# Optimization experiments

Measured on AMD Instinct MI355X. Metric: run time of the kernel, lower is better.

Reference implementation:

```python
import jax, jax.numpy as jnp
import numpy as np

N_HEADS = 12


def setup_inputs() -> dict:
    key = jax.random.key(0)
    ks = jax.random.split(key, 4)
    B, T, C = 1, 4096, 768
    x = jax.random.normal(ks[0], (B, T, C), dtype=jnp.float32)
    w_qkv = jax.random.normal(ks[1], (C, 3 * C), dtype=jnp.float32) * (C ** -0.5)
    b_qkv = jnp.zeros((3 * C,), dtype=jnp.float32)
    w_proj = jax.random.normal(ks[2], (C, C), dtype=jnp.float32) * (C ** -0.5)
    b_proj = jnp.zeros((C,), dtype=jnp.float32)
    return {"x": x, "w_qkv": w_qkv, "b_qkv": b_qkv, "w_proj": w_proj, "b_proj": b_proj}


def reference(x, w_qkv, b_qkv, w_proj, b_proj):
    B, T, C = x.shape
    H = N_HEADS
    hd = C // H
    qkv = x @ w_qkv + b_qkv                      # [B,T,3C]
    q, k, v = jnp.split(qkv, 3, axis=-1)
    # [B,H,T,hd]
    q = q.reshape(B, T, H, hd).transpose(0, 2, 1, 3)
    k = k.reshape(B, T, H, hd).transpose(0, 2, 1, 3)
    v = v.reshape(B, T, H, hd).transpose(0, 2, 1, 3)
    scale = 1.0 / jnp.sqrt(jnp.float32(hd))
    attn = jnp.einsum('bhqd,bhkd->bhqk', q, k) * scale  # [B,H,T,T]
    causal = jnp.tril(jnp.ones((T, T), dtype=bool))
    attn = jnp.where(causal, attn, jnp.float32(-jnp.inf))
    attn = jax.nn.softmax(attn, axis=-1)
    out = jnp.einsum('bhqk,bhkd->bhqd', attn, v)        # [B,H,T,hd]
    out = out.transpose(0, 2, 1, 3).reshape(B, T, C)
    return out @ w_proj + b_proj
```

## Files before the change

### kernel.cpp

```cpp
#include <hip/hip_runtime.h>
#include <hip/hip_bf16.h>


#define T_SEQ 4096
#define C_DIM 768
#define C3    2304
#define NH    12
#define HD    64

typedef __attribute__((ext_vector_type(8))) short bf16x8;
typedef __attribute__((ext_vector_type(4))) short bf16x4;
typedef __attribute__((ext_vector_type(4))) float f32x4;

__device__ inline unsigned short f2bf(float f) {
  union { float f; unsigned u; } v; v.f = f;
  unsigned r = v.u + 0x7fff + ((v.u >> 16) & 1);
  return (unsigned short)(r >> 16);
}
__device__ inline unsigned short f2bf_trunc(float f) {
  union { float f; unsigned u; } v; v.f = f;
  return (unsigned short)(v.u >> 16);
}

__device__ inline void gl2lds16(const void* g, void* l) {
  __builtin_amdgcn_global_load_lds(
      (const __attribute__((address_space(1))) unsigned int*)g,
      (__attribute__((address_space(3))) unsigned int*)l, 16, 0, 0);
}

#if __has_builtin(__builtin_amdgcn_exp2f)
#define EXP2F(x) __builtin_amdgcn_exp2f(x)
#else
#define EXP2F(x) exp2f(x)
#endif

#define NB_CONV  (T_SEQ * C_DIM / 2048)
#define NB_TQKV  ((C3 / 32) * (C_DIM / 32))
#define NB_TPROJ ((C_DIM / 32) * (C_DIM / 32))

__global__ __launch_bounds__(256) void prep_fused(
    const float* __restrict__ x, const float* __restrict__ w_qkv,
    const float* __restrict__ w_proj, unsigned short* __restrict__ xb,
    unsigned short* __restrict__ wqkvT, unsigned short* __restrict__ wprojT) {
  __shared__ float t[32][33];
  const int b = blockIdx.x;
  const int tid = threadIdx.x;

  if (b < NB_CONV) {
    int i = (b * 256 + tid) * 8;
    float4 v0 = *(const float4*)(x + i);
    float4 v1 = *(const float4*)(x + i + 4);
    unsigned short o[8] = {f2bf(v0.x), f2bf(v0.y), f2bf(v0.z), f2bf(v0.w),
                           f2bf(v1.x), f2bf(v1.y), f2bf(v1.z), f2bf(v1.w)};
    *(uint4*)(xb + i) = *(uint4*)o;
    return;
  }
  const float* in;
  unsigned short* outT;
  int R, Cc, bi;
  if (b < NB_CONV + NB_TQKV) {
    in = w_qkv; outT = wqkvT; R = C_DIM; Cc = C3; bi = b - NB_CONV;
  } else {
    in = w_proj; outT = wprojT; R = C_DIM; Cc = C_DIM; bi = b - NB_CONV - NB_TQKV;
  }
  const int tx = tid & 31, ty = tid >> 5;
  const int c0 = (bi % (Cc / 32)) * 32, r0 = (bi / (Cc / 32)) * 32;
#pragma unroll
  for (int i = 0; i < 4; ++i) {
    int r = ty + i * 8;
    t[r][tx] = in[(size_t)(r0 + r) * Cc + c0 + tx];
  }
  __syncthreads();
#pragma unroll
  for (int i = 0; i < 4; ++i) {
    int c = ty + i * 8;
    outT[(size_t)(c0 + c) * R + r0 + tx] = f2bf(t[tx][c]);
  }
}

__global__ __launch_bounds__(512) void gemm_qkv(
    const unsigned short* __restrict__ A, const unsigned short* __restrict__ Bt,
    const float* __restrict__ bias, unsigned short* __restrict__ Cq,
    unsigned short* __restrict__ vTp, int M, int N, int K) {
  __shared__ unsigned short As[256 * 64];
  __shared__ unsigned short Bs[128 * 64];
  const int tid = threadIdx.x;
  const int wave = tid >> 6, lane = tid & 63;
  const int lo = lane & 15, g8 = lane >> 4;
  const int lo7 = lo & 7;
  const int wm = wave >> 1, wn = wave & 1;
  const int bm = blockIdx.y * 256, bn = blockIdx.x * 128;
  const int drow = tid >> 3;
  const int dslot = (tid & 7) * 8;
  const int dsrc = ((tid & 7) ^ (drow & 7)) * 8;

  f32x4 acc[4][4];
#pragma unroll
  for (int mt = 0; mt < 4; ++mt)
#pragma unroll
    for (int nt = 0; nt < 4; ++nt) acc[mt][nt] = (f32x4){0.f, 0.f, 0.f, 0.f};

  const unsigned short* Abase = A + (size_t)bm * K;
  const unsigned short* Bbase = Bt + (size_t)bn * K;

  for (int k0 = 0; k0 < K; k0 += 64) {
    __syncthreads();
#pragma unroll
    for (int p = 0; p < 4; ++p) {
      const int r = p * 64 + drow;
      gl2lds16(Abase + (size_t)r * K + k0 + dsrc, As + r * 64 + dslot);
    }
#pragma unroll
    for (int p = 0; p < 2; ++p) {
      const int r = p * 64 + drow;
      gl2lds16(Bbase + (size_t)r * K + k0 + dsrc, Bs + r * 64 + dslot);
    }
    __syncthreads();

#pragma unroll
    for (int kk = 0; kk < 2; ++kk) {
      bf16x8 a[4], b[4];
#pragma unroll
      for (int mt = 0; mt < 4; ++mt)
        a[mt] = *(const bf16x8*)(
            As + (wm * 64 + mt * 16 + lo) * 64 + (((kk * 4 + g8) ^ lo7) * 8));
#pragma unroll
      for (int nt = 0; nt < 4; ++nt)
        b[nt] = *(const bf16x8*)(
            Bs + (wn * 64 + nt * 16 + lo) * 64 + (((kk * 4 + g8) ^ lo7) * 8));
#pragma unroll
      for (int mt = 0; mt < 4; ++mt)
#pragma unroll
        for (int nt = 0; nt < 4; ++nt)
          acc[mt][nt] = __builtin_amdgcn_mfma_f32_16x16x32_bf16(a[mt], b[nt], acc[mt][nt], 0, 0, 0);
    }
  }

  if (bn < 2 * C_DIM) {
    const float sc = (bn < C_DIM) ? 0.18033688011112042f : 1.0f;
#pragma unroll
    for (int nt = 0; nt < 4; ++nt) {
      const int n = bn + wn * 64 + nt * 16 + lo;
      const float bv = bias[n];
#pragma unroll
      for (int mt = 0; mt < 4; ++mt)
#pragma unroll
        for (int r = 0; r < 4; ++r) {
          const int m = bm + wm * 64 + mt * 16 + g8 * 4 + r;
          Cq[(size_t)m * C3 + n] = f2bf((acc[mt][nt][r] + bv) * sc);
        }
    }
  } else {
#pragma unroll
    for (int nt = 0; nt < 4; ++nt) {
      const int n = bn + wn * 64 + nt * 16 + lo;
      const float bv = bias[n];
      unsigned short* row = vTp + (size_t)(n - 2 * C_DIM) * T_SEQ;
#pragma unroll
      for (int mt = 0; mt < 4; ++mt) {
        const int mbase = (bm + wm * 64 + mt * 16 + g8 * 4) & ~31;
        bf16x4 o4;
#pragma unroll
        for (int r = 0; r < 4; ++r) o4[r] = (short)f2bf(acc[mt][nt][r] + bv);
        *(bf16x4*)(row + mbase + 8 * g8 + 4 * (mt & 1)) = o4;
      }
    }
  }
}

__global__ __launch_bounds__(256) void gemm_bt_mfma(
    const unsigned short* __restrict__ A, const unsigned short* __restrict__ Bt,
    const float* __restrict__ bias, float* __restrict__ C,
    int M, int N, int K) {
  __shared__ unsigned short As[128 * 64];
  __shared__ unsigned short Bs[128 * 64];
  const int tid = threadIdx.x;
  const int wave = tid >> 6, lane = tid & 63;
  const int lo = lane & 15, g8 = lane >> 4;
  const int lo7 = lo & 7;
  const int wm = wave >> 1, wn = wave & 1;
  const int bm = blockIdx.y * 128, bn = blockIdx.x * 128;
  const int drow8 = lane >> 3;
  const int dslot = (lane & 7) * 8;
  const int dsrc = ((lane & 7) ^ drow8) * 8;

  f32x4 acc[4][4];
#pragma unroll
  for (int mt = 0; mt < 4; ++mt)
#pragma unroll
    for (int nt = 0; nt < 4; ++nt) acc[mt][nt] = (f32x4){0.f, 0.f, 0.f, 0.f};

  const unsigned short* Abase = A + (size_t)bm * K;
  const unsigned short* Bbase = Bt + (size_t)bn * K;

  for (int k0 = 0; k0 < K; k0 += 64) {
    __syncthreads();
#pragma unroll
    for (int p = 0; p < 4; ++p) {
      const int r = p * 32 + wave * 8 + drow8;
      gl2lds16(Abase + (size_t)r * K + k0 + dsrc, As + r * 64 + dslot);
      gl2lds16(Bbase + (size_t)r * K + k0 + dsrc, Bs + r * 64 + dslot);
    }
    __syncthreads();

#pragma unroll
    for (int kk = 0; kk < 2; ++kk) {
      bf16x8 a[4], b[4];
#pragma unroll
      for (int mt = 0; mt < 4; ++mt)
        a[mt] = *(const bf16x8*)(
            As + (wm * 64 + mt * 16 + lo) * 64 + (((kk * 4 + g8) ^ lo7) * 8));
#pragma unroll
      for (int nt = 0; nt < 4; ++nt)
        b[nt] = *(const bf16x8*)(
            Bs + (wn * 64 + nt * 16 + lo) * 64 + (((kk * 4 + g8) ^ lo7) * 8));
#pragma unroll
      for (int mt = 0; mt < 4; ++mt)
#pragma unroll
        for (int nt = 0; nt < 4; ++nt)
          acc[mt][nt] = __builtin_amdgcn_mfma_f32_16x16x32_bf16(a[mt], b[nt], acc[mt][nt], 0, 0, 0);
    }
  }

#pragma unroll
  for (int nt = 0; nt < 4; ++nt) {
    const int n = bn + wn * 64 + nt * 16 + lo;
    const float bv = bias[n];
#pragma unroll
    for (int mt = 0; mt < 4; ++mt)
#pragma unroll
      for (int r = 0; r < 4; ++r) {
        const int m = bm + wm * 64 + mt * 16 + g8 * 4 + r;
        C[(size_t)m * N + n] = acc[mt][nt][r] + bv;
      }
  }
}

#define NRECH  51
#define PO_REC (256 * 64)
#define KSTEP  (64 * C3)

__device__ inline int s_pref(int qt) {
  const int A = qt / 3, B = qt - 3 * A;
  return qt + 3 * A * (A - 1) / 2 + A * B;
}

__global__ __launch_bounds__(512, 2) void flash_attn_qb256(
    const unsigned short* __restrict__ qkv,
    const unsigned short* __restrict__ vTp,
    float* __restrict__ Po, float* __restrict__ Pl) {
  __shared__ unsigned short Ks[3][64 * 64];
  __shared__ unsigned short Vs[3][64 * 64];

  const int u = blockIdx.x;
  int h, qt, c, k0, T;
  if (u < 480) {
    h = u / 40;
    const int w40 = u % 40;
    qt = 2; c = 0;
    for (int q = 15; q >= 2; --q) {
      const int A = q / 3, B = q - 3 * A;
      const int F = 3 * A * (A - 1) / 2 + A * (B + 1);
      if (w40 >= F) { qt = q; c = w40 - F; break; }
    }
    k0 = 12 * c; T = 12;
  } else if (u < 540) {
    const int v = u - 480; h = v / 5; const int e = v % 5;
    qt = 3 * e + 1; c = e; k0 = 12 * e; T = 8;
  } else {
    const int v = u - 540; h = v / 6; const int e = v % 6;
    qt = 3 * e; c = e; k0 = 12 * e; T = 4;
  }
  const int rec = h * NRECH + s_pref(qt) + c;
  const int qt4 = 4 * qt;

  const int tid = threadIdx.x;
  const int w = tid >> 6;
  const int lane = tid & 63;
  const int lo = lane & 15;
  const int g = lane >> 4;
  const int lo7 = lo & 7;

  const unsigned short* Kg = qkv + C_DIM + h * HD;
  const unsigned short* Vg = vTp + (size_t)(h * HD) * T_SEQ;

  const int drow = tid >> 3;
  const int dslot = (tid & 7) * 8;
  const int dsrc = ((tid & 7) ^ (drow & 7)) * 8;

  const int qw0 = w * 32 + lo;
  bf16x8 qb[2][2];
#pragma unroll
  for (int qh = 0; qh < 2; ++qh)
#pragma unroll
    for (int dh = 0; dh < 2; ++dh)
      qb[qh][dh] = *(const bf16x8*)(
          qkv + (size_t)(qt * 256 + qw0 + qh * 16) * C3 + h * HD + dh * 32 + g * 8);

  const unsigned short* pK = Kg + (size_t)(k0 * 64 + drow) * C3 + dsrc;
  const unsigned short* pV = Vg + (size_t)drow * T_SEQ + k0 * 64 + dsrc;

  auto stage = [&](int buf) __attribute__((always_inline)) {
    gl2lds16(pK, Ks[buf] + drow * 64 + dslot);
    gl2lds16(pV, Vs[buf] + drow * 64 + dslot);
    pK += KSTEP; pV += 64;
  };

  bf16x8 onesb;
#pragma unroll
  for (int e = 0; e < 8; ++e) onesb[e] = (short)0x3F80;

  stage(0);
  stage(1);
  asm volatile("s_waitcnt vmcnt(2)" ::: "memory");
  __builtin_amdgcn_s_barrier();

  f32x4 o_acc[2][4];
  f32x4 lacc[2];
#pragma unroll
  for (int qh = 0; qh < 2; ++qh) {
    lacc[qh] = (f32x4){0.f, 0.f, 0.f, 0.f};
#pragma unroll
    for (int dt = 0; dt < 4; ++dt) o_acc[qh][dt] = (f32x4){0.f, 0.f, 0.f, 0.f};
  }

  int ic = 0, iw = 2;
  int ktc = k0;
  for (int t = 0; t < T; ++t) {
    if (t + 2 < T) stage(iw);
    const unsigned short* Kc = Ks[ic];
    const unsigned short* Vc = Vs[ic];

    f32x4 st[2][4];
#pragma unroll
    for (int qh = 0; qh < 2; ++qh)
#pragma unroll
      for (int mt = 0; mt < 4; ++mt) st[qh][mt] = (f32x4){0.f, 0.f, 0.f, 0.f};
    __builtin_amdgcn_s_setprio(1);
#pragma unroll
    for (int mt = 0; mt < 4; ++mt)
#pragma unroll
      for (int dh = 0; dh < 2; ++dh) {
        bf16x8 a = *(const bf16x8*)(
            Kc + (mt * 16 + lo) * 64 + (((dh * 4 + g) ^ lo7) * 8));
#pragma unroll
        for (int qh = 0; qh < 2; ++qh)
          st[qh][mt] = __builtin_amdgcn_mfma_f32_16x16x32_bf16(
              a, qb[qh][dh], st[qh][mt], 0, 0, 0);
      }
    __builtin_amdgcn_s_setprio(0);

    if (ktc >= qt4) {
      const int mb = (ktc - qt4) * 64;
#pragma unroll
      for (int qh = 0; qh < 2; ++qh) {
        const int qr = qw0 + qh * 16;
#pragma unroll
        for (int mt = 0; mt < 4; ++mt)
#pragma unroll
          for (int r = 0; r < 4; ++r)
            if (mb + mt * 16 + g * 4 + r > qr) st[qh][mt][r] = -1e30f;
      }
    }

    bf16x8 pt[2][2];
#pragma unroll
    for (int qh = 0; qh < 2; ++qh)
#pragma unroll
      for (int kh = 0; kh < 2; ++kh)
#pragma unroll
        for (int jj = 0; jj < 4; ++jj) {
          float e0 = EXP2F(st[qh][kh * 2][jj]);
          float e1 = EXP2F(st[qh][kh * 2 + 1][jj]);
          pt[qh][kh][jj] = (short)f2bf_trunc(e0);
          pt[qh][kh][4 + jj] = (short)f2bf_trunc(e1);
        }

    __builtin_amdgcn_s_setprio(1);
#pragma unroll
    for (int qh = 0; qh < 2; ++qh) {
      lacc[qh] = __builtin_amdgcn_mfma_f32_16x16x32_bf16(onesb, pt[qh][0], lacc[qh], 0, 0, 0);
      lacc[qh] = __builtin_amdgcn_mfma_f32_16x16x32_bf16(onesb, pt[qh][1], lacc[qh], 0, 0, 0);
    }
#pragma unroll
    for (int dt = 0; dt < 4; ++dt)
#pragma unroll
      for (int kh = 0; kh < 2; ++kh) {
        bf16x8 av = *(const bf16x8*)(
            Vc + (dt * 16 + lo) * 64 + (((kh * 4 + g) ^ lo7) * 8));
#pragma unroll
        for (int qh = 0; qh < 2; ++qh)
          o_acc[qh][dt] = __builtin_amdgcn_mfma_f32_16x16x32_bf16(
              av, pt[qh][kh], o_acc[qh][dt], 0, 0, 0);
      }
    __builtin_amdgcn_s_setprio(0);

    if (t + 2 < T)
      asm volatile("s_waitcnt vmcnt(2)" ::: "memory");
    else
      asm volatile("s_waitcnt vmcnt(0)" ::: "memory");
    __builtin_amdgcn_s_barrier();

    ic = (ic == 2) ? 0 : ic + 1;
    iw = (iw == 2) ? 0 : iw + 1;
    ++ktc;
  }

  float* PoS = Po + (size_t)rec * PO_REC;
#pragma unroll
  for (int qh = 0; qh < 2; ++qh)
#pragma unroll
    for (int dt = 0; dt < 4; ++dt)
      *(f32x4*)(PoS + (qw0 + qh * 16) * 64 + dt * 16 + g * 4) = o_acc[qh][dt];
  if (g == 0) {
    float* PlS = Pl + (size_t)rec * 256;
#pragma unroll
    for (int qh = 0; qh < 2; ++qh) PlS[qw0 + qh * 16] = lacc[qh][0];
  }
}

__global__ __launch_bounds__(256) void combine_qb256(
    const float* __restrict__ Po, const float* __restrict__ Pl,
    unsigned short* __restrict__ out) {
  const int bid = blockIdx.x;
  const int h = bid >> 4, qt = bid & 15;
  const int nc = qt / 3 + 1;
  const int rec0 = h * NRECH + s_pref(qt);
  const int tid = threadIdx.x;
  const int q0 = tid >> 2;
  const int c0 = (tid & 3) * 16;
#pragma unroll
  for (int qq = 0; qq < 4; ++qq) {
    const int q = qq * 64 + q0;
    float l = 0.f;
    f32x4 acc[4];
#pragma unroll
    for (int e = 0; e < 4; ++e) acc[e] = (f32x4){0.f, 0.f, 0.f, 0.f};
    for (int c = 0; c < nc; ++c) {
      const size_t base = (size_t)(rec0 + c);
      l += Pl[base * 256 + q];
      const float* P = Po + base * PO_REC + q * 64 + c0;
#pragma unroll
      for (int e = 0; e < 4; ++e) acc[e] += *(const f32x4*)(P + e * 4);
    }
    const float inv = 1.0f / l;
    unsigned short ob[16];
#pragma unroll
    for (int e = 0; e < 4; ++e)
#pragma unroll
      for (int r = 0; r < 4; ++r) ob[e * 4 + r] = f2bf(acc[e][r] * inv);
    unsigned short* op = out + (size_t)(qt * 256 + q) * C_DIM + h * 64 + c0;
    *(uint4*)op = *(uint4*)ob;
    *(uint4*)(op + 8) = *(uint4*)(ob + 8);
  }
}

extern "C" void kernel_launch(void* const* d_in, const int* in_sizes, int n_in,
                              void* d_out, int out_size, void* d_ws, size_t ws_size,
                              hipStream_t stream) {
  const float* x      = (const float*)d_in[0];
  const float* w_qkv  = (const float*)d_in[1];
  const float* b_qkv  = (const float*)d_in[2];
  const float* w_proj = (const float*)d_in[3];
  const float* b_proj = (const float*)d_in[4];
  float* out = (float*)d_out;

  unsigned short* xb     = (unsigned short*)d_ws;
  unsigned short* wqkvT  = xb + (size_t)T_SEQ * C_DIM;
  unsigned short* wprojT = wqkvT + (size_t)C3 * C_DIM;
  unsigned short* qkv    = wprojT + (size_t)C_DIM * C_DIM;
  unsigned short* vTp    = qkv + (size_t)T_SEQ * C3;
  unsigned short* attnb  = xb;
  float* Po = (float*)(vTp + (size_t)C_DIM * T_SEQ);
  float* Pl = Po + (size_t)NH * NRECH * PO_REC;

  prep_fused<<<NB_CONV + NB_TQKV + NB_TPROJ, 256, 0, stream>>>(
      x, w_qkv, w_proj, xb, wqkvT, wprojT);

  gemm_qkv<<<dim3(C3 / 128, T_SEQ / 256), 512, 0, stream>>>(
      xb, wqkvT, b_qkv, qkv, vTp, T_SEQ, C3, C_DIM);

  flash_attn_qb256<<<612, 512, 0, stream>>>(qkv, vTp, Po, Pl);

  combine_qb256<<<NH * 16, 256, 0, stream>>>(Po, Pl, attnb);

  gemm_bt_mfma<<<dim3(C_DIM / 128, T_SEQ / 128), 256, 0, stream>>>(
      attnb, wprojT, b_proj, out, T_SEQ, C_DIM, C_DIM);
}
```

Measured before the change: 174.6 us.

## Split key tile across wave pairs in flash attention with LDS reduction

Reorganizes the attention kernel so each pair of waves shares a 64-query group and splits the 64-key tile in halves. Each wave now holds 4 query subtiles and does half the K/V work per tile, replacing the ones-matrix MFMA row-sum with scalar accumulation plus cross-lane shuffles. The partial outputs of the two waves are merged through LDS in four serialized rounds at the end. The combine kernel is split into twice as many blocks. The trade-off is more accumulator registers (launch bounds no longer force 2 blocks per CU) and extra reduction syncs at the end, in exchange for fewer K fragment loads and less redundant work.

```diff
diff --git a/kernel.cpp b/kernel.cpp
--- a/kernel.cpp
+++ b/kernel.cpp
@@ -245,7 +245,7 @@
   return qt + 3 * A * (A - 1) / 2 + A * B;
 }
 
-__global__ __launch_bounds__(512, 2) void flash_attn_qb256(
+__global__ __launch_bounds__(512) void flash_attn_ksplit(
     const unsigned short* __restrict__ qkv,
     const unsigned short* __restrict__ vTp,
     float* __restrict__ Po, float* __restrict__ Pl) {
@@ -276,6 +276,8 @@
 
   const int tid = threadIdx.x;
   const int w = tid >> 6;
+  const int qg = w >> 1;
+  const int kg = w & 1;
   const int lane = tid & 63;
   const int lo = lane & 15;
   const int g = lane >> 4;
@@ -288,14 +290,13 @@
   const int dslot = (tid & 7) * 8;
   const int dsrc = ((tid & 7) ^ (drow & 7)) * 8;
 
-  const int qw0 = w * 32 + lo;
-  bf16x8 qb[2][2];
-#pragma unroll
-  for (int qh = 0; qh < 2; ++qh)
+  bf16x8 qb[4][2];
+#pragma unroll
+  for (int qh = 0; qh < 4; ++qh)
 #pragma unroll
     for (int dh = 0; dh < 2; ++dh)
       qb[qh][dh] = *(const bf16x8*)(
-          qkv + (size_t)(qt * 256 + qw0 + qh * 16) * C3 + h * HD + dh * 32 + g * 8);
+          qkv + (size_t)(qt * 256 + qg * 64 + qh * 16 + lo) * C3 + h * HD + dh * 32 + g * 8);
 
   const unsigned short* pK = Kg + (size_t)(k0 * 64 + drow) * C3 + dsrc;
   const unsigned short* pV = Vg + (size_t)drow * T_SEQ + k0 * 64 + dsrc;
@@ -306,20 +307,16 @@
     pK += KSTEP; pV += 64;
   };
 
-  bf16x8 onesb;
-#pragma unroll
-  for (int e = 0; e < 8; ++e) onesb[e] = (short)0x3F80;
-
   stage(0);
   stage(1);
   asm volatile("s_waitcnt vmcnt(2)" ::: "memory");
   __builtin_amdgcn_s_barrier();
 
-  f32x4 o_acc[2][4];
-  f32x4 lacc[2];
-#pragma unroll
-  for (int qh = 0; qh < 2; ++qh) {
-    lacc[qh] = (f32x4){0.f, 0.f, 0.f, 0.f};
+  f32x4 o_acc[4][4];
+  float l_i[4];
+#pragma unroll
+  for (int qh = 0; qh < 4; ++qh) {
+    l_i[qh] = 0.f;
 #pragma unroll
     for (int dt = 0; dt < 4; ++dt) o_acc[qh][dt] = (f32x4){0.f, 0.f, 0.f, 0.f};
   }
@@ -331,68 +328,55 @@
     const unsigned short* Kc = Ks[ic];
     const unsigned short* Vc = Vs[ic];
 
-    f32x4 st[2][4];
-#pragma unroll
-    for (int qh = 0; qh < 2; ++qh)
-#pragma unroll
-      for (int mt = 0; mt < 4; ++mt) st[qh][mt] = (f32x4){0.f, 0.f, 0.f, 0.f};
+    bf16x8 af[2][2], av[4];
+#pragma unroll
+    for (int mt = 0; mt < 2; ++mt)
+#pragma unroll
+      for (int dh = 0; dh < 2; ++dh)
+        af[mt][dh] = *(const bf16x8*)(
+            Kc + (kg * 32 + mt * 16 + lo) * 64 + (((dh * 4 + g) ^ lo7) * 8));
+#pragma unroll
+    for (int dt = 0; dt < 4; ++dt)
+      av[dt] = *(const bf16x8*)(
+          Vc + (dt * 16 + lo) * 64 + (((kg * 4 + g) ^ lo7) * 8));
+
+    const bool diag = (ktc >= qt4);
+    const int mb = (ktc - qt4) * 64 + kg * 32;
+
     __builtin_amdgcn_s_setprio(1);
 #pragma unroll
-    for (int mt = 0; mt < 4; ++mt)
+    for (int qh = 0; qh < 4; ++qh) {
+      f32x4 st0 = (f32x4){0.f, 0.f, 0.f, 0.f};
+      f32x4 st1 = (f32x4){0.f, 0.f, 0.f, 0.f};
 #pragma unroll
       for (int dh = 0; dh < 2; ++dh) {
-        bf16x8 a = *(const bf16x8*)(
-            Kc + (mt * 16 + lo) * 64 + (((dh * 4 + g) ^ lo7) * 8));
-#pragma unroll
-        for (int qh = 0; qh < 2; ++qh)
-          st[qh][mt] = __builtin_amdgcn_mfma_f32_16x16x32_bf16(
-              a, qb[qh][dh], st[qh][mt], 0, 0, 0);
-      }
-    __builtin_amdgcn_s_setprio(0);
-
-    if (ktc >= qt4) {
-      const int mb = (ktc - qt4) * 64;
-#pragma unroll
-      for (int qh = 0; qh < 2; ++qh) {
-        const int qr = qw0 + qh * 16;
-#pragma unroll
-        for (int mt = 0; mt < 4; ++mt)
-#pragma unroll
-          for (int r = 0; r < 4; ++r)
-            if (mb + mt * 16 + g * 4 + r > qr) st[qh][mt][r] = -1e30f;
-      }
-    }
-
-    bf16x8 pt[2][2];
-#pragma unroll
-    for (int qh = 0; qh < 2; ++qh)
-#pragma unroll
-      for (int kh = 0; kh < 2; ++kh)
-#pragma unroll
-        for (int jj = 0; jj < 4; ++jj) {
-          float e0 = EXP2F(st[qh][kh * 2][jj]);
-          float e1 = EXP2F(st[qh][kh * 2 + 1][jj]);
-          pt[qh][kh][jj] = (short)f2bf_trunc(e0);
-          pt[qh][kh][4 + jj] = (short)f2bf_trunc(e1);
+        st0 = __builtin_amdgcn_mfma_f32_16x16x32_bf16(af[0][dh], qb[qh][dh], st0, 0, 0, 0);
+        st1 = __builtin_amdgcn_mfma_f32_16x16x32_bf16(af[1][dh], qb[qh][dh], st1, 0, 0, 0);
+      }
+      if (diag) {
+        const int qr = qg * 64 + qh * 16 + lo;
+#pragma unroll
+        for (int r = 0; r < 4; ++r) {
+          if (mb + g * 4 + r > qr) st0[r] = -1e30f;
+          if (mb + 16 + g * 4 + r > qr) st1[r] = -1e30f;
         }
-
-    __builtin_amdgcn_s_setprio(1);
-#pragma unroll
-    for (int qh = 0; qh < 2; ++qh) {
-      lacc[qh] = __builtin_amdgcn_mfma_f32_16x16x32_bf16(onesb, pt[qh][0], lacc[qh], 0, 0, 0);
-      lacc[qh] = __builtin_amdgcn_mfma_f32_16x16x32_bf16(onesb, pt[qh][1], lacc[qh], 0, 0, 0);
-    }
-#pragma unroll
-    for (int dt = 0; dt < 4; ++dt)
-#pragma unroll
-      for (int kh = 0; kh < 2; ++kh) {
-        bf16x8 av = *(const bf16x8*)(
-            Vc + (dt * 16 + lo) * 64 + (((kh * 4 + g) ^ lo7) * 8));
-#pragma unroll
-        for (int qh = 0; qh < 2; ++qh)
-          o_acc[qh][dt] = __builtin_amdgcn_mfma_f32_16x16x32_bf16(
-              av, pt[qh][kh], o_acc[qh][dt], 0, 0, 0);
-      }
+      }
+      bf16x8 pb;
+      float ls = 0.f;
+#pragma unroll
+      for (int jj = 0; jj < 4; ++jj) {
+        float e0 = EXP2F(st0[jj]);
+        float e1 = EXP2F(st1[jj]);
+        ls += e0 + e1;
+        pb[jj] = (short)f2bf_trunc(e0);
+        pb[4 + jj] = (short)f2bf_trunc(e1);
+      }
+      l_i[qh] += ls;
+#pragma unroll
+      for (int dt = 0; dt < 4; ++dt)
+        o_acc[qh][dt] = __builtin_amdgcn_mfma_f32_16x16x32_bf16(
+            av[dt], pb, o_acc[qh][dt], 0, 0, 0);
+    }
     __builtin_amdgcn_s_setprio(0);
 
     if (t + 2 < T)
@@ -406,16 +390,51 @@
     ++ktc;
   }
 
-  float* PoS = Po + (size_t)rec * PO_REC;
-#pragma unroll
-  for (int qh = 0; qh < 2; ++qh)
-#pragma unroll
-    for (int dt = 0; dt < 4; ++dt)
-      *(f32x4*)(PoS + (qw0 + qh * 16) * 64 + dt * 16 + g * 4) = o_acc[qh][dt];
-  if (g == 0) {
-    float* PlS = Pl + (size_t)rec * 256;
-#pragma unroll
-    for (int qh = 0; qh < 2; ++qh) PlS[qw0 + qh * 16] = lacc[qh][0];
+#pragma unroll
+  for (int qh = 0; qh < 4; ++qh) {
+    l_i[qh] += __shfl_xor(l_i[qh], 16);
+    l_i[qh] += __shfl_xor(l_i[qh], 32);
+  }
+  float* red = (float*)Ks[0];
+#pragma unroll
+  for (int p = 0; p < 4; ++p) {
+    if (qg == p && kg == 1) {
+#pragma unroll
+      for (int qh = 0; qh < 4; ++qh) {
+#pragma unroll
+        for (int dt = 0; dt < 4; ++dt)
+          *(f32x4*)(red + (qh * 16 + lo) * 64 + dt * 16 + g * 4) = o_acc[qh][dt];
+        if (g == 0) red[4096 + qh * 16 + lo] = l_i[qh];
+      }
+    }
+    __syncthreads();
+    if (qg == p && kg == 0) {
+#pragma unroll
+      for (int qh = 0; qh < 4; ++qh) {
+#pragma unroll
+        for (int dt = 0; dt < 4; ++dt) {
+          f32x4 v = *(const f32x4*)(red + (qh * 16 + lo) * 64 + dt * 16 + g * 4);
+          o_acc[qh][dt] += v;
+        }
+        l_i[qh] += red[4096 + qh * 16 + lo];
+      }
+    }
+    __syncthreads();
+  }
+
+  if (kg == 0) {
+    float* PoS = Po + (size_t)rec * PO_REC;
+#pragma unroll
+    for (int qh = 0; qh < 4; ++qh)
+#pragma unroll
+      for (int dt = 0; dt < 4; ++dt)
+        *(f32x4*)(PoS + (qg * 64 + qh * 16 + lo) * 64 + dt * 16 + g * 4) =
+            o_acc[qh][dt];
+    if (g == 0) {
+      float* PlS = Pl + (size_t)rec * 256;
+#pragma unroll
+      for (int qh = 0; qh < 4; ++qh) PlS[qg * 64 + qh * 16 + lo] = l_i[qh];
+    }
   }
 }
 
@@ -423,15 +442,17 @@
     const float* __restrict__ Po, const float* __restrict__ Pl,
     unsigned short* __restrict__ out) {
   const int bid = blockIdx.x;
-  const int h = bid >> 4, qt = bid & 15;
+  const int h = bid / 32;
+  const int r2 = bid % 32;
+  const int qt = r2 >> 1, half = r2 & 1;
   const int nc = qt / 3 + 1;
   const int rec0 = h * NRECH + s_pref(qt);
   const int tid = threadIdx.x;
   const int q0 = tid >> 2;
   const int c0 = (tid & 3) * 16;
 #pragma unroll
-  for (int qq = 0; qq < 4; ++qq) {
-    const int q = qq * 64 + q0;
+  for (int qq = 0; qq < 2; ++qq) {
+    const int q = (half * 2 + qq) * 64 + q0;
     float l = 0.f;
     f32x4 acc[4];
 #pragma unroll
@@ -480,9 +501,9 @@
   gemm_qkv<<<dim3(C3 / 128, T_SEQ / 256), 512, 0, stream>>>(
       xb, wqkvT, b_qkv, qkv, vTp, T_SEQ, C3, C_DIM);
 
-  flash_attn_qb256<<<612, 512, 0, stream>>>(qkv, vTp, Po, Pl);
-
-  combine_qb256<<<NH * 16, 256, 0, stream>>>(Po, Pl, attnb);
+  flash_attn_ksplit<<<612, 512, 0, stream>>>(qkv, vTp, Po, Pl);
+
+  combine_qb256<<<NH * 16 * 2, 256, 0, stream>>>(Po, Pl, attnb);
 
   gemm_bt_mfma<<<dim3(C_DIM / 128, T_SEQ / 128), 256, 0, stream>>>(
       attnb, wprojT, b_proj, out, T_SEQ, C_DIM, C_DIM);
```

Result: slower. 195.5 us (+11.9%).

## Fuse split-K combine into flash attention via last-block atomic counter

Applied to the files above, without the earlier changes.

Removes the separate combine kernel launch: each attention block writes its partial output and row sum, then bumps a per-(head, query-tile) atomic counter. The last block to finish for that tile reduces all partials, normalises, and writes the bf16 attention output. Counters are zeroed in the prep kernel. This saves a launch and its serialization gap, at the cost of threadfences, an atomic, and a reduction tail on the last-arriving blocks.

```diff
diff --git a/kernel.cpp b/kernel.cpp
--- a/kernel.cpp
+++ b/kernel.cpp
@@ -41,12 +41,14 @@
 __global__ __launch_bounds__(256) void prep_fused(
     const float* __restrict__ x, const float* __restrict__ w_qkv,
     const float* __restrict__ w_proj, unsigned short* __restrict__ xb,
-    unsigned short* __restrict__ wqkvT, unsigned short* __restrict__ wprojT) {
+    unsigned short* __restrict__ wqkvT, unsigned short* __restrict__ wprojT,
+    unsigned int* __restrict__ cnt) {
   __shared__ float t[32][33];
   const int b = blockIdx.x;
   const int tid = threadIdx.x;
 
   if (b < NB_CONV) {
+    if (b == 0 && tid < NH * 16) cnt[tid] = 0;
     int i = (b * 256 + tid) * 8;
     float4 v0 = *(const float4*)(x + i);
     float4 v1 = *(const float4*)(x + i + 4);
@@ -248,9 +250,12 @@
 __global__ __launch_bounds__(512, 2) void flash_attn_qb256(
     const unsigned short* __restrict__ qkv,
     const unsigned short* __restrict__ vTp,
-    float* __restrict__ Po, float* __restrict__ Pl) {
+    float* __restrict__ Po, float* __restrict__ Pl,
+    unsigned short* __restrict__ outb,
+    unsigned int* __restrict__ cnt) {
   __shared__ unsigned short Ks[3][64 * 64];
   __shared__ unsigned short Vs[3][64 * 64];
+  __shared__ unsigned int lastv;
 
   const int u = blockIdx.x;
   int h, qt, c, k0, T;
@@ -406,52 +411,54 @@
     ++ktc;
   }
 
-  float* PoS = Po + (size_t)rec * PO_REC;
-#pragma unroll
-  for (int qh = 0; qh < 2; ++qh)
-#pragma unroll
-    for (int dt = 0; dt < 4; ++dt)
-      *(f32x4*)(PoS + (qw0 + qh * 16) * 64 + dt * 16 + g * 4) = o_acc[qh][dt];
-  if (g == 0) {
-    float* PlS = Pl + (size_t)rec * 256;
-#pragma unroll
-    for (int qh = 0; qh < 2; ++qh) PlS[qw0 + qh * 16] = lacc[qh][0];
-  }
-}
-
-__global__ __launch_bounds__(256) void combine_qb256(
-    const float* __restrict__ Po, const float* __restrict__ Pl,
-    unsigned short* __restrict__ out) {
-  const int bid = blockIdx.x;
-  const int h = bid >> 4, qt = bid & 15;
+  {
+    float* PoS = Po + (size_t)rec * PO_REC;
+#pragma unroll
+    for (int qh = 0; qh < 2; ++qh)
+#pragma unroll
+      for (int dt = 0; dt < 4; ++dt)
+        *(f32x4*)(PoS + (qw0 + qh * 16) * 64 + dt * 16 + g * 4) = o_acc[qh][dt];
+    if (g == 0) {
+      float* PlS = Pl + (size_t)rec * 256;
+#pragma unroll
+      for (int qh = 0; qh < 2; ++qh) PlS[qw0 + qh * 16] = lacc[qh][0];
+    }
+  }
+
   const int nc = qt / 3 + 1;
-  const int rec0 = h * NRECH + s_pref(qt);
-  const int tid = threadIdx.x;
-  const int q0 = tid >> 2;
-  const int c0 = (tid & 3) * 16;
-#pragma unroll
-  for (int qq = 0; qq < 4; ++qq) {
-    const int q = qq * 64 + q0;
+  __threadfence();
+  __syncthreads();
+  if (tid == 0) lastv = atomicAdd(&cnt[h * 16 + qt], 1u);
+  __syncthreads();
+  if (lastv == (unsigned)(nc - 1)) {
+    __threadfence();
+    const int rec0 = h * NRECH + s_pref(qt);
+    const int q = tid >> 1;
+    const int c0 = (tid & 1) * 32;
     float l = 0.f;
-    f32x4 acc[4];
-#pragma unroll
-    for (int e = 0; e < 4; ++e) acc[e] = (f32x4){0.f, 0.f, 0.f, 0.f};
-    for (int c = 0; c < nc; ++c) {
-      const size_t base = (size_t)(rec0 + c);
+#pragma unroll
+    for (int qh = 0; qh < 2; ++qh)
+#pragma unroll
+      for (int dt = 0; dt < 4; ++dt) o_acc[qh][dt] = (f32x4){0.f, 0.f, 0.f, 0.f};
+    for (int cc = 0; cc < nc; ++cc) {
+      const size_t base = (size_t)(rec0 + cc);
       l += Pl[base * 256 + q];
       const float* P = Po + base * PO_REC + q * 64 + c0;
 #pragma unroll
-      for (int e = 0; e < 4; ++e) acc[e] += *(const f32x4*)(P + e * 4);
+      for (int e = 0; e < 8; ++e)
+        o_acc[e >> 2][e & 3] += *(const f32x4*)(P + e * 4);
     }
     const float inv = 1.0f / l;
-    unsigned short ob[16];
-#pragma unroll
-    for (int e = 0; e < 4; ++e)
-#pragma unroll
-      for (int r = 0; r < 4; ++r) ob[e * 4 + r] = f2bf(acc[e][r] * inv);
-    unsigned short* op = out + (size_t)(qt * 256 + q) * C_DIM + h * 64 + c0;
-    *(uint4*)op = *(uint4*)ob;
-    *(uint4*)(op + 8) = *(uint4*)(ob + 8);
+    unsigned short ob[32];
+#pragma unroll
+    for (int e = 0; e < 8; ++e)
+#pragma unroll
+      for (int r = 0; r < 4; ++r)
+        ob[e * 4 + r] = f2bf(o_acc[e >> 2][e & 3][r] * inv);
+    unsigned short* op = outb + (size_t)(qt * 256 + q) * C_DIM + h * 64 + c0;
+#pragma unroll
+    for (int e2 = 0; e2 < 4; ++e2)
+      *(uint4*)(op + e2 * 8) = *(uint4*)(ob + e2 * 8);
   }
 }
 
@@ -473,16 +480,15 @@
   unsigned short* attnb  = xb;
   float* Po = (float*)(vTp + (size_t)C_DIM * T_SEQ);
   float* Pl = Po + (size_t)NH * NRECH * PO_REC;
+  unsigned int* cnt = (unsigned int*)(Pl + (size_t)NH * NRECH * 256);
 
   prep_fused<<<NB_CONV + NB_TQKV + NB_TPROJ, 256, 0, stream>>>(
-      x, w_qkv, w_proj, xb, wqkvT, wprojT);
+      x, w_qkv, w_proj, xb, wqkvT, wprojT, cnt);
 
   gemm_qkv<<<dim3(C3 / 128, T_SEQ / 256), 512, 0, stream>>>(
       xb, wqkvT, b_qkv, qkv, vTp, T_SEQ, C3, C_DIM);
 
-  flash_attn_qb256<<<612, 512, 0, stream>>>(qkv, vTp, Po, Pl);
-
-  combine_qb256<<<NH * 16, 256, 0, stream>>>(Po, Pl, attnb);
+  flash_attn_qb256<<<612, 512, 0, stream>>>(qkv, vTp, Po, Pl, attnb, cnt);
 
   gemm_bt_mfma<<<dim3(C_DIM / 128, T_SEQ / 128), 256, 0, stream>>>(
       attnb, wprojT, b_proj, out, T_SEQ, C_DIM, C_DIM);
```

After: 422.8 us. 2.42x slower.
